# Performance work log

Hardware: AMD Instinct MI355X
Metric: run time of the kernel (lower is better)

The kernel has to match this reference:

```python
import jax
import jax.numpy as jnp
import numpy as np
from jax import lax

TAU = 1.0
EPS = 1e-20


def setup_inputs() -> dict:
    key = jax.random.key(0)
    ks = jax.random.split(key, 8)
    B, n, M, G = 256, 128, 512, 512  # batch, seq, mem_size, global dim
    SLOTS = 15                        # his_mem slots (mem_slots - 1)
    d_q = M + G
    his_mem = jax.random.normal(ks[0], (B, SLOTS, M), dtype=jnp.float32)
    states = jax.random.normal(ks[1], (B, n, M), dtype=jnp.float32)
    states_mask = jnp.round(jax.random.uniform(ks[2], (B, n), dtype=jnp.float32))
    global_trace = jax.random.normal(ks[3], (B, G), dtype=jnp.float32)
    null_mem = jnp.zeros((B, 1, M), dtype=jnp.float32)
    gumbel_u = jax.random.uniform(ks[4], (B, n, SLOTS + 1), dtype=jnp.float32)
    attn_W = jax.random.normal(ks[5], (M, d_q + M), dtype=jnp.float32) * 0.02
    attn_b = jax.random.normal(ks[6], (M,), dtype=jnp.float32) * 0.02
    stdv = 1.0 / np.sqrt(M)
    v = jax.random.normal(ks[7], (M,), dtype=jnp.float32) * stdv
    return {"his_mem": his_mem, "states": states, "states_mask": states_mask,
            "global_trace": global_trace, "null_mem": null_mem,
            "gumbel_u": gumbel_u, "attn_W": attn_W, "attn_b": attn_b, "v": v}


def _gumbel_softmax_hard(logits, u, tau):
    # deterministic gumbel noise from uniform samples u in [0,1)
    g = -jnp.log(-jnp.log(jnp.clip(u, EPS, 1.0)) + EPS)
    y_soft = jax.nn.softmax((logits + g) / tau, axis=-1)
    y_hard = jax.nn.one_hot(jnp.argmax(y_soft, axis=-1), logits.shape[-1],
                            dtype=y_soft.dtype)
    # straight-through estimator (matches torch F.gumbel_softmax hard=True)
    return y_hard - lax.stop_gradient(y_soft) + y_soft


def _forward(his_mem, states, states_mask, global_trace, null_mem,
             gumbel_u, attn_W, attn_b, v):
    B, n, M = states.shape
    S = his_mem.shape[1] + 1  # mem_slots (including null slot)

    def step(hm, xs):
        state, mask, u = xs  # [B,M], [B], [B,S]
        mem = jnp.concatenate([hm, null_mem], axis=1)          # [B,S,M]
        query = jnp.concatenate([state, global_trace], axis=1)  # [B,d_q]
        q = jnp.broadcast_to(query[:, None, :], (B, S, query.shape[-1]))
        energy = jnp.tanh(jnp.concatenate([q, mem], axis=2) @ attn_W.T + attn_b)
        attn_energies = energy @ v                              # [B,S]
        attn_weights = jax.nn.softmax(attn_energies, axis=-1)
        empty_mask = (jnp.sum(jnp.abs(mem), axis=-1) == 0).astype(attn_weights.dtype)
        attn_weights = attn_weights + empty_mask * 10.0
        slot_select = _gumbel_softmax_hard(attn_weights, u, TAU)  # [B,S]
        write_mask = (slot_select[:, : S - 1] * mask[:, None])[:, :, None]  # [B,S-1,1]
        hm = (1.0 - write_mask) * hm + write_mask * state[:, None, :]
        return hm, slot_select

    xs = (jnp.swapaxes(states, 0, 1),        # [n,B,M]
          jnp.swapaxes(states_mask, 0, 1),   # [n,B]
          jnp.swapaxes(gumbel_u, 0, 1))      # [n,B,S]
    hm_final, log = lax.scan(step, his_mem, xs)
    write_log = jnp.swapaxes(log, 0, 1)      # [B,n,S]
    return hm_final, write_log


def reference(his_mem, states, states_mask, global_trace, null_mem,
              gumbel_u, attn_W, attn_b, v):
    return _forward(his_mem, states, states_mask, global_trace, null_mem,
                    gumbel_u, attn_W, attn_b, v)
```

## Files before the change

### kernel.cpp

```cpp
#include <hip/hip_runtime.h>

constexpr int kB = 256;
constexpr int kN = 128;
constexpr int kM = 512;
constexpr int kSlots = 15;
constexpr int kS = 16;
constexpr int kW = 1536;
constexpr int kCap = 8192;

__device__ __forceinline__ float tanh_fast(float x)
{
    float xc = fminf(15.f, fmaxf(-15.f, x));
    float ex = __expf(2.f * xc);
    return 1.f - 2.f * __builtin_amdgcn_rcpf(ex + 1.f);
}

__global__ __launch_bounds__(256) void prep1_k(
    const float* __restrict__ his_mem, const float* __restrict__ null_mem,
    const float* __restrict__ gumbel_u, float* __restrict__ out,
    int* __restrict__ empty0, int* __restrict__ cnt, int* __restrict__ total,
    unsigned* __restrict__ list, int* __restrict__ listPos,
    int* __restrict__ ambBatch, unsigned char* __restrict__ amb_flags)
{
    const int b = blockIdx.x;
    const int tid = threadIdx.x;
    const int wave = tid >> 6, lane = tid & 63;
    __shared__ int eflag[kS];
    float* out_hm = out;
    float* out_log = out + (size_t)kB * kSlots * kM;

    for (int s = wave; s < kS; s += 4) {
        const float* p = (s < kSlots) ? his_mem + (size_t)(b * kSlots + s) * kM
                                      : null_mem + (size_t)b * kM;
        float4 v0 = *(const float4*)(p + lane * 4);
        float4 v1 = *(const float4*)(p + 256 + lane * 4);
        int nz = (v0.x != 0.f) | (v0.y != 0.f) | (v0.z != 0.f) | (v0.w != 0.f) |
                 (v1.x != 0.f) | (v1.y != 0.f) | (v1.z != 0.f) | (v1.w != 0.f);
        unsigned long long bal = __ballot(nz);
        if (lane == 0) eflag[s] = (bal == 0ull) ? 1 : 0;
        if (s < kSlots) {
            float* dst = out_hm + (size_t)(b * kSlots + s) * kM;
            *(float4*)(dst + lane * 4) = v0;
            *(float4*)(dst + 256 + lane * 4) = v1;
        }
    }
    __syncthreads();
    if (tid < kS) empty0[b * kS + tid] = eflag[tid];

    if (tid < kN) {
        const int idx = b * kN + tid;
        const float* up = gumbel_u + (size_t)idx * kS;
        float g[kS];
#pragma unroll
        for (int s = 0; s < kS; ++s) {
            float u = fminf(fmaxf(up[s], 1e-20f), 1.0f);
            g[s] = -logf(-logf(u) + 1e-20f);
        }
        float rhs = g[15] + 10.f * (eflag[15] ? 1.f : 0.f) - 1.01f;
        bool amb = false;
#pragma unroll
        for (int s = 0; s < kSlots; ++s)
            amb = amb || (g[s] + 10.f * (eflag[s] ? 1.f : 0.f) >= rhs);
        amb_flags[idx] = amb ? 1 : 0;
        if (amb) {
            int pos = atomicAdd(&total[0], 1);
            if (pos < kCap) list[pos] = (unsigned)idx;
            listPos[idx] = pos;
            int prev = atomicAdd(&cnt[b], 1);
            if (prev == 0) {
                int bp = atomicAdd(&total[1], 1);
                ambBatch[bp] = b;
            }
        }
        float* lp = out_log + (size_t)idx * kS;
        float4 zz = make_float4(0.f, 0.f, 0.f, 0.f);
        *(float4*)(lp + 0) = zz;
        *(float4*)(lp + 4) = zz;
        *(float4*)(lp + 8) = zz;
        *(float4*)(lp + 12) = make_float4(0.f, 0.f, 0.f, 1.f);
    }
}

__global__ __launch_bounds__(256) void prep2_k(
    const float* __restrict__ W, const float* __restrict__ his_mem,
    const float* __restrict__ null_mem, const float* __restrict__ states,
    const float* __restrict__ global_trace, const float* __restrict__ attn_b,
    const int* __restrict__ total, const int* __restrict__ ambBatch,
    const unsigned* __restrict__ list, float* __restrict__ C0,
    float* __restrict__ qCache, float* __restrict__ cwCache,
    int* __restrict__ stepNz)
{
    const int tid = threadIdx.x;

    if (blockIdx.x < 512) {
        const int nab = total[1];
        const int cx = blockIdx.x >> 3;
        const int cy = blockIdx.x & 7;
        if (cx * 4 >= nab) return;
        __shared__ float As[16 * 68];
        __shared__ float Bs[16 * 68];
        const int n0 = cy * 64;
        const int row_l = tid >> 2;
        const int k4 = (tid & 3) * 4;
        const int ty = tid >> 4, tx = tid & 15;

        int bi = cx * 4 + (row_l >> 4);
        if (bi >= nab) bi = nab - 1;
        const int b = ambBatch[bi];
        const int s = row_l & 15;
        const float* ap = (s < kSlots) ? (his_mem + (size_t)(b * kSlots + s) * kM)
                                       : (null_mem + (size_t)b * kM);
        const float* wp = W + (size_t)(n0 + row_l) * kW + 1024;

        float acc[4][4];
#pragma unroll
        for (int i = 0; i < 4; ++i)
#pragma unroll
            for (int j = 0; j < 4; ++j) acc[i][j] = 0.f;

        for (int kt = 0; kt < kM; kt += 16) {
            float4 a4 = *(const float4*)(ap + kt + k4);
            float4 b4 = *(const float4*)(wp + kt + k4);
            __syncthreads();
            As[(k4 + 0) * 68 + row_l] = a4.x; As[(k4 + 1) * 68 + row_l] = a4.y;
            As[(k4 + 2) * 68 + row_l] = a4.z; As[(k4 + 3) * 68 + row_l] = a4.w;
            Bs[(k4 + 0) * 68 + row_l] = b4.x; Bs[(k4 + 1) * 68 + row_l] = b4.y;
            Bs[(k4 + 2) * 68 + row_l] = b4.z; Bs[(k4 + 3) * 68 + row_l] = b4.w;
            __syncthreads();
#pragma unroll
            for (int k = 0; k < 16; ++k) {
                const float4 av = *(const float4*)&As[k * 68 + ty * 4];
                const float4 bv = *(const float4*)&Bs[k * 68 + tx * 4];
                acc[0][0] = fmaf(av.x, bv.x, acc[0][0]);
                acc[0][1] = fmaf(av.x, bv.y, acc[0][1]);
                acc[0][2] = fmaf(av.x, bv.z, acc[0][2]);
                acc[0][3] = fmaf(av.x, bv.w, acc[0][3]);
                acc[1][0] = fmaf(av.y, bv.x, acc[1][0]);
                acc[1][1] = fmaf(av.y, bv.y, acc[1][1]);
                acc[1][2] = fmaf(av.y, bv.z, acc[1][2]);
                acc[1][3] = fmaf(av.y, bv.w, acc[1][3]);
                acc[2][0] = fmaf(av.z, bv.x, acc[2][0]);
                acc[2][1] = fmaf(av.z, bv.y, acc[2][1]);
                acc[2][2] = fmaf(av.z, bv.z, acc[2][2]);
                acc[2][3] = fmaf(av.z, bv.w, acc[2][3]);
                acc[3][0] = fmaf(av.w, bv.x, acc[3][0]);
                acc[3][1] = fmaf(av.w, bv.y, acc[3][1]);
                acc[3][2] = fmaf(av.w, bv.z, acc[3][2]);
                acc[3][3] = fmaf(av.w, bv.w, acc[3][3]);
            }
        }
#pragma unroll
        for (int i = 0; i < 4; ++i) {
            int rl = ty * 4 + i;
            int bij = cx * 4 + (rl >> 4);
            if (bij >= nab) bij = nab - 1;
            int ro = ambBatch[bij] * kS + (rl & 15);
            float4 o = make_float4(acc[i][0], acc[i][1], acc[i][2], acc[i][3]);
            *(float4*)(C0 + (size_t)ro * kM + n0 + tx * 4) = o;
        }
    } else {
        int n = total[0];
        if (n > kCap) n = kCap;
        __shared__ float Xs[1024];
        __shared__ int nzs;

        for (int c = (int)blockIdx.x - 512; c < n * 16; c += 2048) {
            const int i = c >> 4;
            const int j = c & 15;
            const int idx = (int)list[i];
            const int b = idx >> 7;
            __syncthreads();
            if (tid == 0) nzs = 0;
            __syncthreads();
            float s0 = states[(size_t)idx * kM + tid];
            float s1 = states[(size_t)idx * kM + 256 + tid];
            Xs[tid] = s0; Xs[256 + tid] = s1;
            Xs[512 + tid] = global_trace[(size_t)b * kM + tid];
            Xs[768 + tid] = global_trace[(size_t)b * kM + 256 + tid];
            if (s0 != 0.f || s1 != 0.f) nzs = 1;
            __syncthreads();

            const int g = tid >> 4;
            const int l = tid & 15;
#pragma unroll
            for (int p = 0; p < 2; ++p) {
                const int r = j * 32 + p * 16 + g;
                const float* wr = W + (size_t)r * kW;
                float accq = 0.f, accc = 0.f;
#pragma unroll
                for (int jj = 0; jj < 16; ++jj) {
                    int k = l * 4 + jj * 64;
                    float4 w4 = *(const float4*)(wr + k);
                    float4 x4 = *(const float4*)&Xs[k];
                    accq = fmaf(w4.x, x4.x, accq); accq = fmaf(w4.y, x4.y, accq);
                    accq = fmaf(w4.z, x4.z, accq); accq = fmaf(w4.w, x4.w, accq);
                }
#pragma unroll
                for (int jj = 0; jj < 8; ++jj) {
                    int k = l * 4 + jj * 64;
                    float4 w4 = *(const float4*)(wr + 1024 + k);
                    float4 x4 = *(const float4*)&Xs[k];
                    accc = fmaf(w4.x, x4.x, accc); accc = fmaf(w4.y, x4.y, accc);
                    accc = fmaf(w4.z, x4.z, accc); accc = fmaf(w4.w, x4.w, accc);
                }
                accq += __shfl_xor(accq, 1); accq += __shfl_xor(accq, 2);
                accq += __shfl_xor(accq, 4); accq += __shfl_xor(accq, 8);
                accc += __shfl_xor(accc, 1); accc += __shfl_xor(accc, 2);
                accc += __shfl_xor(accc, 4); accc += __shfl_xor(accc, 8);
                if (l == 0) {
                    qCache[(size_t)i * kM + r] = accq + attn_b[r];
                    cwCache[(size_t)i * kM + r] = accc;
                }
            }
            if (tid == 0 && j == 0) stepNz[i] = nzs;
        }
    }
}

constexpr int kCsStride = 528;

__global__ __launch_bounds__(256) void phaseB_k(
    const float* __restrict__ C0, const int* __restrict__ empty0,
    const unsigned char* __restrict__ amb_flags, const int* __restrict__ cnt,
    const int* __restrict__ listPos, const float* __restrict__ qCache,
    const float* __restrict__ cwCache, const int* __restrict__ stepNz,
    const float* __restrict__ states, const float* __restrict__ states_mask,
    const float* __restrict__ gumbel_u, const float* __restrict__ global_trace,
    const float* __restrict__ W, const float* __restrict__ attn_b,
    const float* __restrict__ v, float* __restrict__ out)
{
    const int b = blockIdx.x;
    if (cnt[b] == 0) return;
    const int tid = threadIdx.x;
    float* out_hm = out;
    float* out_log = out + (size_t)kB * kSlots * kM;

    __shared__ float Cs[kS * kCsStride];
    __shared__ float Xb[1024];
    __shared__ float Qb[kM];
    __shared__ float vs[kM];
    __shared__ float e_sh[kS];
    __shared__ float empty_sh[kS];
    __shared__ unsigned char flS[kN];
    __shared__ int slot_src[kSlots];
    __shared__ int k_sh, wk_sh, nz_sh;

    for (int i = tid; i < kS * kM; i += 256) {
        int s = i >> 9, m = i & 511;
        Cs[s * kCsStride + m] = C0[(size_t)(b * kS + s) * kM + m];
    }
    for (int i = tid; i < kM; i += 256) {
        vs[i] = v[i];
        Xb[512 + i] = global_trace[(size_t)b * kM + i];
    }
    if (tid < kS) empty_sh[tid] = empty0[b * kS + tid] ? 1.0f : 0.0f;
    if (tid < kSlots) slot_src[tid] = -1;
    if (tid < kN) flS[tid] = amb_flags[b * kN + tid];
    __syncthreads();

    const int sidx = tid >> 4;
    const int ml = tid & 15;

    for (int t = 0; t < kN; ++t) {
        if (!flS[t]) continue;

        const int pos = listPos[b * kN + t];
        const float* qp;
        if (pos < kCap) {
            qp = qCache + (size_t)pos * kM;
        } else {
            Xb[tid] = states[(size_t)(b * kN + t) * kM + tid];
            Xb[256 + tid] = states[(size_t)(b * kN + t) * kM + 256 + tid];
            __syncthreads();
            const int g2 = tid >> 4, l2 = tid & 15;
            for (int r0 = 0; r0 < kM; r0 += 16) {
                int r = r0 + g2;
                const float* wr = W + (size_t)r * kW;
                float a = 0.f;
                for (int k = l2 * 4; k < 1024; k += 64) {
                    float4 w4 = *(const float4*)(wr + k);
                    float4 x4 = *(const float4*)&Xb[k];
                    a = fmaf(w4.x, x4.x, a); a = fmaf(w4.y, x4.y, a);
                    a = fmaf(w4.z, x4.z, a); a = fmaf(w4.w, x4.w, a);
                }
                a += __shfl_xor(a, 1); a += __shfl_xor(a, 2);
                a += __shfl_xor(a, 4); a += __shfl_xor(a, 8);
                if (l2 == 0) Qb[r] = a + attn_b[r];
            }
            __syncthreads();
            qp = Qb;
        }

        const float* crow = &Cs[sidx * kCsStride];
        float acc = 0.f;
#pragma unroll
        for (int j = 0; j < 8; ++j) {
            int m = ml * 4 + j * 64;
            float4 q4 = *(const float4*)(qp + m);
            float4 c4 = *(const float4*)&crow[m];
            float4 v4 = *(const float4*)&vs[m];
            acc = fmaf(v4.x, tanh_fast(q4.x + c4.x), acc);
            acc = fmaf(v4.y, tanh_fast(q4.y + c4.y), acc);
            acc = fmaf(v4.z, tanh_fast(q4.z + c4.z), acc);
            acc = fmaf(v4.w, tanh_fast(q4.w + c4.w), acc);
        }
        acc += __shfl_xor(acc, 1); acc += __shfl_xor(acc, 2);
        acc += __shfl_xor(acc, 4); acc += __shfl_xor(acc, 8);
        if (ml == 0) e_sh[sidx] = acc;
        __syncthreads();

        if (tid < 64) {
            int s = tid;
            float ev = (s < kS) ? e_sh[s] : -3.0e38f;
            float mx = ev;
            mx = fmaxf(mx, __shfl_xor(mx, 1));
            mx = fmaxf(mx, __shfl_xor(mx, 2));
            mx = fmaxf(mx, __shfl_xor(mx, 4));
            mx = fmaxf(mx, __shfl_xor(mx, 8));
            float w = (s < kS) ? __expf(ev - mx) : 0.f;
            float sm = w;
            sm += __shfl_xor(sm, 1); sm += __shfl_xor(sm, 2);
            sm += __shfl_xor(sm, 4); sm += __shfl_xor(sm, 8);
            w = w / sm;
            w += 10.0f * ((s < kS) ? empty_sh[s] : 0.f);
            float z;
            if (s < kS) {
                float u = gumbel_u[(size_t)(b * kN + t) * kS + s];
                u = fminf(fmaxf(u, 1e-20f), 1.0f);
                float g = -logf(-logf(u) + 1e-20f);
                z = w + g;
            } else z = -3.0e38f;
            float zm = z;
            zm = fmaxf(zm, __shfl_xor(zm, 1));
            zm = fmaxf(zm, __shfl_xor(zm, 2));
            zm = fmaxf(zm, __shfl_xor(zm, 4));
            zm = fmaxf(zm, __shfl_xor(zm, 8));
            unsigned long long bal = __ballot(z == zm) & 0xFFFFull;
            if (s == 0) k_sh = __ffsll(bal) - 1;
        }
        __syncthreads();

        const int k = k_sh;
        if (tid < kS) out_log[(size_t)(b * kN + t) * kS + tid] = (tid == k) ? 1.f : 0.f;
        if (tid == 0) {
            float mv = states_mask[b * kN + t];
            wk_sh = (k < kSlots && mv != 0.0f) ? k : -1;
            nz_sh = 0;
        }
        __syncthreads();

        const int wk = wk_sh;
        if (wk >= 0) {
            if (pos < kCap) {
                Cs[wk * kCsStride + tid] = cwCache[(size_t)pos * kM + tid];
                Cs[wk * kCsStride + 256 + tid] = cwCache[(size_t)pos * kM + 256 + tid];
                if (tid == 0) {
                    slot_src[wk] = t;
                    empty_sh[wk] = stepNz[pos] ? 0.f : 1.f;
                }
            } else {
                if (Xb[tid] != 0.f || Xb[256 + tid] != 0.f) nz_sh = 1;
                __syncthreads();
                const int g2 = tid >> 4, l2 = tid & 15;
                for (int r0 = 0; r0 < kM; r0 += 16) {
                    int r = r0 + g2;
                    const float* wr = W + (size_t)r * kW + 1024;
                    float ca = 0.f;
                    for (int k2 = l2 * 4; k2 < kM; k2 += 64) {
                        float4 w4 = *(const float4*)(wr + k2);
                        float4 x4 = *(const float4*)&Xb[k2];
                        ca = fmaf(w4.x, x4.x, ca); ca = fmaf(w4.y, x4.y, ca);
                        ca = fmaf(w4.z, x4.z, ca); ca = fmaf(w4.w, x4.w, ca);
                    }
                    ca += __shfl_xor(ca, 1); ca += __shfl_xor(ca, 2);
                    ca += __shfl_xor(ca, 4); ca += __shfl_xor(ca, 8);
                    if (l2 == 0) Cs[wk * kCsStride + r] = ca;
                }
                __syncthreads();
                if (tid == 0) {
                    slot_src[wk] = t;
                    empty_sh[wk] = nz_sh ? 0.f : 1.f;
                }
            }
        }
        __syncthreads();
    }

    for (int s = 0; s < kSlots; ++s) {
        int ts = slot_src[s];
        if (ts >= 0) {
            float* dst = out_hm + (size_t)(b * kSlots + s) * kM;
            dst[tid] = states[(size_t)(b * kN + ts) * kM + tid];
            dst[tid + 256] = states[(size_t)(b * kN + ts) * kM + tid + 256];
        }
    }
}

extern "C" void kernel_launch(void* const* d_in, const int* in_sizes, int n_in,
                              void* d_out, int out_size, void* d_ws, size_t ws_size,
                              hipStream_t stream)
{
    const float* his_mem      = (const float*)d_in[0];
    const float* states       = (const float*)d_in[1];
    const float* states_mask  = (const float*)d_in[2];
    const float* global_trace = (const float*)d_in[3];
    const float* null_mem     = (const float*)d_in[4];
    const float* gumbel_u     = (const float*)d_in[5];
    const float* attn_W       = (const float*)d_in[6];
    const float* attn_b       = (const float*)d_in[7];
    const float* v            = (const float*)d_in[8];

    float* C0 = (float*)d_ws;
    float* qCache = C0 + (size_t)kB * kS * kM;
    float* cwCache = qCache + (size_t)kCap * kM;
    int* cnt = (int*)(cwCache + (size_t)kCap * kM);
    int* total = cnt + kB;
    int* empty0 = total + 16;
    int* ambBatch = empty0 + kB * kS;
    int* stepNz = ambBatch + kB;
    int* listPos = stepNz + kCap;
    unsigned* list = (unsigned*)(listPos + kB * kN);
    unsigned char* amb = (unsigned char*)(list + kB * kN);

    hipMemsetAsync(cnt, 0, (kB + 16) * sizeof(int), stream);
    prep1_k<<<kB, 256, 0, stream>>>(his_mem, null_mem, gumbel_u, (float*)d_out,
                                    empty0, cnt, total, list, listPos, ambBatch,
                                    amb);
    prep2_k<<<2560, 256, 0, stream>>>(attn_W, his_mem, null_mem, states,
                                      global_trace, attn_b, total, ambBatch,
                                      list, C0, qCache, cwCache, stepNz);
    phaseB_k<<<kB, 256, 0, stream>>>(C0, empty0, amb, cnt, listPos, qCache,
                                     cwCache, stepNz, states, states_mask,
                                     gumbel_u, global_trace, attn_W, attn_b, v,
                                     (float*)d_out);
}
```

Measured before the change: 170.4 us.

## Fuse prep kernels and sequential scan into one per-batch kernel

Collapses the three-kernel pipeline (memset, prep1, batched GEMM/precompute prep2, sequential phaseB) into a single kernel with one block per batch element. Each block builds its ambiguous-step list in shared memory via ballots instead of global atomics. It computes the memory-projection C0 from shared-memory copies of the slots, and computes the query and written-slot projections inline per ambiguous step rather than caching them in global workspace. This removes launch overhead and global round trips, but puts all per-step matvec work on only 256 blocks in sequence rather than spreading it across a wide parallel grid.

```diff
diff --git a/kernel.cpp b/kernel.cpp
--- a/kernel.cpp
+++ b/kernel.cpp
@@ -6,7 +6,8 @@
 constexpr int kSlots = 15;
 constexpr int kS = 16;
 constexpr int kW = 1536;
-constexpr int kCap = 8192;
+constexpr int kMsStride = 520;
+constexpr int kCsStride = 528;
 
 __device__ __forceinline__ float tanh_fast(float x)
 {
@@ -15,38 +16,53 @@
     return 1.f - 2.f * __builtin_amdgcn_rcpf(ex + 1.f);
 }
 
-__global__ __launch_bounds__(256) void prep1_k(
-    const float* __restrict__ his_mem, const float* __restrict__ null_mem,
-    const float* __restrict__ gumbel_u, float* __restrict__ out,
-    int* __restrict__ empty0, int* __restrict__ cnt, int* __restrict__ total,
-    unsigned* __restrict__ list, int* __restrict__ listPos,
-    int* __restrict__ ambBatch, unsigned char* __restrict__ amb_flags)
+__global__ __launch_bounds__(256) void fused_k(
+    const float* __restrict__ his_mem, const float* __restrict__ states,
+    const float* __restrict__ states_mask, const float* __restrict__ global_trace,
+    const float* __restrict__ null_mem, const float* __restrict__ gumbel_u,
+    const float* __restrict__ W, const float* __restrict__ attn_b,
+    const float* __restrict__ v, float* __restrict__ out)
 {
     const int b = blockIdx.x;
     const int tid = threadIdx.x;
     const int wave = tid >> 6, lane = tid & 63;
-    __shared__ int eflag[kS];
+
+    __shared__ __align__(16) float Ms[kS * kMsStride];
+    __shared__ __align__(16) float Cs[kS * kCsStride];
+    __shared__ __align__(16) float Xq[1024];
+    __shared__ __align__(16) float Qs[kM];
+    __shared__ __align__(16) float vs[kM];
+    __shared__ __align__(16) float bs[kM];
+    __shared__ float empty_p[kS];
+    __shared__ float e_sh[kS];
+    __shared__ unsigned char ambList[kN];
+    __shared__ int wcnt[2];
+    __shared__ int slot_src[kSlots];
+    __shared__ int cnt_sh, k_sh, wk_sh, nz_sh;
+
     float* out_hm = out;
     float* out_log = out + (size_t)kB * kSlots * kM;
 
     for (int s = wave; s < kS; s += 4) {
-        const float* p = (s < kSlots) ? his_mem + (size_t)(b * kSlots + s) * kM
+        const float* p = (s < kSlots) ? his_mem + ((size_t)b * kSlots + s) * kM
                                       : null_mem + (size_t)b * kM;
         float4 v0 = *(const float4*)(p + lane * 4);
         float4 v1 = *(const float4*)(p + 256 + lane * 4);
+        *(float4*)&Ms[s * kMsStride + lane * 4] = v0;
+        *(float4*)&Ms[s * kMsStride + 256 + lane * 4] = v1;
         int nz = (v0.x != 0.f) | (v0.y != 0.f) | (v0.z != 0.f) | (v0.w != 0.f) |
                  (v1.x != 0.f) | (v1.y != 0.f) | (v1.z != 0.f) | (v1.w != 0.f);
         unsigned long long bal = __ballot(nz);
-        if (lane == 0) eflag[s] = (bal == 0ull) ? 1 : 0;
+        if (lane == 0) empty_p[s] = (bal == 0ull) ? 1.f : 0.f;
         if (s < kSlots) {
-            float* dst = out_hm + (size_t)(b * kSlots + s) * kM;
+            float* dst = out_hm + ((size_t)b * kSlots + s) * kM;
             *(float4*)(dst + lane * 4) = v0;
             *(float4*)(dst + 256 + lane * 4) = v1;
         }
     }
     __syncthreads();
-    if (tid < kS) empty0[b * kS + tid] = eflag[tid];
-
+
+    bool amb = false;
     if (tid < kN) {
         const int idx = b * kN + tid;
         const float* up = gumbel_u + (size_t)idx * kS;
@@ -56,22 +72,10 @@
             float u = fminf(fmaxf(up[s], 1e-20f), 1.0f);
             g[s] = -logf(-logf(u) + 1e-20f);
         }
-        float rhs = g[15] + 10.f * (eflag[15] ? 1.f : 0.f) - 1.01f;
-        bool amb = false;
+        float rhs = g[15] + 10.f * empty_p[15] - 1.01f;
 #pragma unroll
         for (int s = 0; s < kSlots; ++s)
-            amb = amb || (g[s] + 10.f * (eflag[s] ? 1.f : 0.f) >= rhs);
-        amb_flags[idx] = amb ? 1 : 0;
-        if (amb) {
-            int pos = atomicAdd(&total[0], 1);
-            if (pos < kCap) list[pos] = (unsigned)idx;
-            listPos[idx] = pos;
-            int prev = atomicAdd(&cnt[b], 1);
-            if (prev == 0) {
-                int bp = atomicAdd(&total[1], 1);
-                ambBatch[bp] = b;
-            }
-        }
+            amb = amb || (g[s] + 10.f * empty_p[s] >= rhs);
         float* lp = out_log + (size_t)idx * kS;
         float4 zz = make_float4(0.f, 0.f, 0.f, 0.f);
         *(float4*)(lp + 0) = zz;
@@ -79,234 +83,124 @@
         *(float4*)(lp + 8) = zz;
         *(float4*)(lp + 12) = make_float4(0.f, 0.f, 0.f, 1.f);
     }
-}
-
-__global__ __launch_bounds__(256) void prep2_k(
-    const float* __restrict__ W, const float* __restrict__ his_mem,
-    const float* __restrict__ null_mem, const float* __restrict__ states,
-    const float* __restrict__ global_trace, const float* __restrict__ attn_b,
-    const int* __restrict__ total, const int* __restrict__ ambBatch,
-    const unsigned* __restrict__ list, float* __restrict__ C0,
-    float* __restrict__ qCache, float* __restrict__ cwCache,
-    int* __restrict__ stepNz)
-{
-    const int tid = threadIdx.x;
-
-    if (blockIdx.x < 512) {
-        const int nab = total[1];
-        const int cx = blockIdx.x >> 3;
-        const int cy = blockIdx.x & 7;
-        if (cx * 4 >= nab) return;
-        __shared__ float As[16 * 68];
-        __shared__ float Bs[16 * 68];
-        const int n0 = cy * 64;
-        const int row_l = tid >> 2;
-        const int k4 = (tid & 3) * 4;
-        const int ty = tid >> 4, tx = tid & 15;
-
-        int bi = cx * 4 + (row_l >> 4);
-        if (bi >= nab) bi = nab - 1;
-        const int b = ambBatch[bi];
-        const int s = row_l & 15;
-        const float* ap = (s < kSlots) ? (his_mem + (size_t)(b * kSlots + s) * kM)
-                                       : (null_mem + (size_t)b * kM);
-        const float* wp = W + (size_t)(n0 + row_l) * kW + 1024;
-
-        float acc[4][4];
-#pragma unroll
-        for (int i = 0; i < 4; ++i)
-#pragma unroll
-            for (int j = 0; j < 4; ++j) acc[i][j] = 0.f;
-
-        for (int kt = 0; kt < kM; kt += 16) {
-            float4 a4 = *(const float4*)(ap + kt + k4);
-            float4 b4 = *(const float4*)(wp + kt + k4);
-            __syncthreads();
-            As[(k4 + 0) * 68 + row_l] = a4.x; As[(k4 + 1) * 68 + row_l] = a4.y;
-            As[(k4 + 2) * 68 + row_l] = a4.z; As[(k4 + 3) * 68 + row_l] = a4.w;
-            Bs[(k4 + 0) * 68 + row_l] = b4.x; Bs[(k4 + 1) * 68 + row_l] = b4.y;
-            Bs[(k4 + 2) * 68 + row_l] = b4.z; Bs[(k4 + 3) * 68 + row_l] = b4.w;
-            __syncthreads();
-#pragma unroll
-            for (int k = 0; k < 16; ++k) {
-                const float4 av = *(const float4*)&As[k * 68 + ty * 4];
-                const float4 bv = *(const float4*)&Bs[k * 68 + tx * 4];
-                acc[0][0] = fmaf(av.x, bv.x, acc[0][0]);
-                acc[0][1] = fmaf(av.x, bv.y, acc[0][1]);
-                acc[0][2] = fmaf(av.x, bv.z, acc[0][2]);
-                acc[0][3] = fmaf(av.x, bv.w, acc[0][3]);
-                acc[1][0] = fmaf(av.y, bv.x, acc[1][0]);
-                acc[1][1] = fmaf(av.y, bv.y, acc[1][1]);
-                acc[1][2] = fmaf(av.y, bv.z, acc[1][2]);
-                acc[1][3] = fmaf(av.y, bv.w, acc[1][3]);
-                acc[2][0] = fmaf(av.z, bv.x, acc[2][0]);
-                acc[2][1] = fmaf(av.z, bv.y, acc[2][1]);
-                acc[2][2] = fmaf(av.z, bv.z, acc[2][2]);
-                acc[2][3] = fmaf(av.z, bv.w, acc[2][3]);
-                acc[3][0] = fmaf(av.w, bv.x, acc[3][0]);
-                acc[3][1] = fmaf(av.w, bv.y, acc[3][1]);
-                acc[3][2] = fmaf(av.w, bv.z, acc[3][2]);
-                acc[3][3] = fmaf(av.w, bv.w, acc[3][3]);
-            }
-        }
-#pragma unroll
-        for (int i = 0; i < 4; ++i) {
-            int rl = ty * 4 + i;
-            int bij = cx * 4 + (rl >> 4);
-            if (bij >= nab) bij = nab - 1;
-            int ro = ambBatch[bij] * kS + (rl & 15);
-            float4 o = make_float4(acc[i][0], acc[i][1], acc[i][2], acc[i][3]);
-            *(float4*)(C0 + (size_t)ro * kM + n0 + tx * 4) = o;
-        }
-    } else {
-        int n = total[0];
-        if (n > kCap) n = kCap;
-        __shared__ float Xs[1024];
-        __shared__ int nzs;
-
-        for (int c = (int)blockIdx.x - 512; c < n * 16; c += 2048) {
-            const int i = c >> 4;
-            const int j = c & 15;
-            const int idx = (int)list[i];
-            const int b = idx >> 7;
-            __syncthreads();
-            if (tid == 0) nzs = 0;
-            __syncthreads();
+    unsigned long long m = __ballot(amb);
+    if (tid < kN && (tid & 63) == 0) wcnt[tid >> 6] = __popcll(m);
+    __syncthreads();
+    if (tid < kN && amb) {
+        int base = (tid >= 64) ? wcnt[0] : 0;
+        int pos = base + __popcll(m & ((1ull << (tid & 63)) - 1ull));
+        ambList[pos] = (unsigned char)tid;
+    }
+    if (tid == 0) cnt_sh = wcnt[0] + wcnt[1];
+    if (tid < kSlots) slot_src[tid] = -1;
+    __syncthreads();
+    const int cnt = cnt_sh;
+    if (cnt == 0) return;
+
+    for (int i = tid; i < kM; i += 256) {
+        vs[i] = v[i];
+        bs[i] = attn_b[i];
+        Xq[512 + i] = global_trace[(size_t)b * kM + i];
+    }
+
+    {
+        const int g = tid >> 4, l = tid & 15;
+        const int koff = l * 4;
+        float4 w4[8];
+        {
+            const float* wr = W + (size_t)g * kW + 1024;
+#pragma unroll
+            for (int jj = 0; jj < 8; ++jj)
+                w4[jj] = *(const float4*)(wr + koff + jj * 64);
+        }
+        for (int r0 = 0; r0 < kM; r0 += 16) {
+            float4 wn[8];
+            if (r0 + 16 < kM) {
+                const float* wr = W + (size_t)(r0 + 16 + g) * kW + 1024;
+#pragma unroll
+                for (int jj = 0; jj < 8; ++jj)
+                    wn[jj] = *(const float4*)(wr + koff + jj * 64);
+            }
+            const int r = r0 + g;
+#pragma unroll
+            for (int s = 0; s < kS; ++s) {
+                const float* ms = &Ms[s * kMsStride + koff];
+                float a0 = 0.f, a1 = 0.f, a2 = 0.f, a3 = 0.f;
+#pragma unroll
+                for (int jj = 0; jj < 8; ++jj) {
+                    float4 m4 = *(const float4*)(ms + jj * 64);
+                    a0 = fmaf(w4[jj].x, m4.x, a0);
+                    a1 = fmaf(w4[jj].y, m4.y, a1);
+                    a2 = fmaf(w4[jj].z, m4.z, a2);
+                    a3 = fmaf(w4[jj].w, m4.w, a3);
+                }
+                float a = (a0 + a1) + (a2 + a3);
+                a += __shfl_xor(a, 1); a += __shfl_xor(a, 2);
+                a += __shfl_xor(a, 4); a += __shfl_xor(a, 8);
+                if (l == s) Cs[s * kCsStride + r] = a;
+            }
+#pragma unroll
+            for (int jj = 0; jj < 8; ++jj) w4[jj] = wn[jj];
+        }
+    }
+    __syncthreads();
+
+    const int sidx = tid >> 4;
+    const int ml = tid & 15;
+    const int g = tid >> 4, l = tid & 15;
+    const int koff = l * 4;
+
+    for (int jj = 0; jj < cnt; ++jj) {
+        const int t = ambList[jj];
+        const int idx = b * kN + t;
+
+        if (tid == 0) nz_sh = 0;
+        __syncthreads();
+        {
             float s0 = states[(size_t)idx * kM + tid];
             float s1 = states[(size_t)idx * kM + 256 + tid];
-            Xs[tid] = s0; Xs[256 + tid] = s1;
-            Xs[512 + tid] = global_trace[(size_t)b * kM + tid];
-            Xs[768 + tid] = global_trace[(size_t)b * kM + 256 + tid];
-            if (s0 != 0.f || s1 != 0.f) nzs = 1;
-            __syncthreads();
-
-            const int g = tid >> 4;
-            const int l = tid & 15;
-#pragma unroll
-            for (int p = 0; p < 2; ++p) {
-                const int r = j * 32 + p * 16 + g;
-                const float* wr = W + (size_t)r * kW;
-                float accq = 0.f, accc = 0.f;
-#pragma unroll
-                for (int jj = 0; jj < 16; ++jj) {
-                    int k = l * 4 + jj * 64;
-                    float4 w4 = *(const float4*)(wr + k);
-                    float4 x4 = *(const float4*)&Xs[k];
-                    accq = fmaf(w4.x, x4.x, accq); accq = fmaf(w4.y, x4.y, accq);
-                    accq = fmaf(w4.z, x4.z, accq); accq = fmaf(w4.w, x4.w, accq);
-                }
-#pragma unroll
-                for (int jj = 0; jj < 8; ++jj) {
-                    int k = l * 4 + jj * 64;
-                    float4 w4 = *(const float4*)(wr + 1024 + k);
-                    float4 x4 = *(const float4*)&Xs[k];
-                    accc = fmaf(w4.x, x4.x, accc); accc = fmaf(w4.y, x4.y, accc);
-                    accc = fmaf(w4.z, x4.z, accc); accc = fmaf(w4.w, x4.w, accc);
-                }
-                accq += __shfl_xor(accq, 1); accq += __shfl_xor(accq, 2);
-                accq += __shfl_xor(accq, 4); accq += __shfl_xor(accq, 8);
-                accc += __shfl_xor(accc, 1); accc += __shfl_xor(accc, 2);
-                accc += __shfl_xor(accc, 4); accc += __shfl_xor(accc, 8);
-                if (l == 0) {
-                    qCache[(size_t)i * kM + r] = accq + attn_b[r];
-                    cwCache[(size_t)i * kM + r] = accc;
-                }
-            }
-            if (tid == 0 && j == 0) stepNz[i] = nzs;
-        }
-    }
-}
-
-constexpr int kCsStride = 528;
-
-__global__ __launch_bounds__(256) void phaseB_k(
-    const float* __restrict__ C0, const int* __restrict__ empty0,
-    const unsigned char* __restrict__ amb_flags, const int* __restrict__ cnt,
-    const int* __restrict__ listPos, const float* __restrict__ qCache,
-    const float* __restrict__ cwCache, const int* __restrict__ stepNz,
-    const float* __restrict__ states, const float* __restrict__ states_mask,
-    const float* __restrict__ gumbel_u, const float* __restrict__ global_trace,
-    const float* __restrict__ W, const float* __restrict__ attn_b,
-    const float* __restrict__ v, float* __restrict__ out)
-{
-    const int b = blockIdx.x;
-    if (cnt[b] == 0) return;
-    const int tid = threadIdx.x;
-    float* out_hm = out;
-    float* out_log = out + (size_t)kB * kSlots * kM;
-
-    __shared__ float Cs[kS * kCsStride];
-    __shared__ float Xb[1024];
-    __shared__ float Qb[kM];
-    __shared__ float vs[kM];
-    __shared__ float e_sh[kS];
-    __shared__ float empty_sh[kS];
-    __shared__ unsigned char flS[kN];
-    __shared__ int slot_src[kSlots];
-    __shared__ int k_sh, wk_sh, nz_sh;
-
-    for (int i = tid; i < kS * kM; i += 256) {
-        int s = i >> 9, m = i & 511;
-        Cs[s * kCsStride + m] = C0[(size_t)(b * kS + s) * kM + m];
-    }
-    for (int i = tid; i < kM; i += 256) {
-        vs[i] = v[i];
-        Xb[512 + i] = global_trace[(size_t)b * kM + i];
-    }
-    if (tid < kS) empty_sh[tid] = empty0[b * kS + tid] ? 1.0f : 0.0f;
-    if (tid < kSlots) slot_src[tid] = -1;
-    if (tid < kN) flS[tid] = amb_flags[b * kN + tid];
-    __syncthreads();
-
-    const int sidx = tid >> 4;
-    const int ml = tid & 15;
-
-    for (int t = 0; t < kN; ++t) {
-        if (!flS[t]) continue;
-
-        const int pos = listPos[b * kN + t];
-        const float* qp;
-        if (pos < kCap) {
-            qp = qCache + (size_t)pos * kM;
-        } else {
-            Xb[tid] = states[(size_t)(b * kN + t) * kM + tid];
-            Xb[256 + tid] = states[(size_t)(b * kN + t) * kM + 256 + tid];
-            __syncthreads();
-            const int g2 = tid >> 4, l2 = tid & 15;
-            for (int r0 = 0; r0 < kM; r0 += 16) {
-                int r = r0 + g2;
-                const float* wr = W + (size_t)r * kW;
-                float a = 0.f;
-                for (int k = l2 * 4; k < 1024; k += 64) {
-                    float4 w4 = *(const float4*)(wr + k);
-                    float4 x4 = *(const float4*)&Xb[k];
-                    a = fmaf(w4.x, x4.x, a); a = fmaf(w4.y, x4.y, a);
-                    a = fmaf(w4.z, x4.z, a); a = fmaf(w4.w, x4.w, a);
-                }
-                a += __shfl_xor(a, 1); a += __shfl_xor(a, 2);
-                a += __shfl_xor(a, 4); a += __shfl_xor(a, 8);
-                if (l2 == 0) Qb[r] = a + attn_b[r];
-            }
-            __syncthreads();
-            qp = Qb;
-        }
-
-        const float* crow = &Cs[sidx * kCsStride];
-        float acc = 0.f;
-#pragma unroll
-        for (int j = 0; j < 8; ++j) {
-            int m = ml * 4 + j * 64;
-            float4 q4 = *(const float4*)(qp + m);
-            float4 c4 = *(const float4*)&crow[m];
-            float4 v4 = *(const float4*)&vs[m];
-            acc = fmaf(v4.x, tanh_fast(q4.x + c4.x), acc);
-            acc = fmaf(v4.y, tanh_fast(q4.y + c4.y), acc);
-            acc = fmaf(v4.z, tanh_fast(q4.z + c4.z), acc);
-            acc = fmaf(v4.w, tanh_fast(q4.w + c4.w), acc);
-        }
-        acc += __shfl_xor(acc, 1); acc += __shfl_xor(acc, 2);
-        acc += __shfl_xor(acc, 4); acc += __shfl_xor(acc, 8);
-        if (ml == 0) e_sh[sidx] = acc;
+            Xq[tid] = s0; Xq[256 + tid] = s1;
+            if (s0 != 0.f || s1 != 0.f) nz_sh = 1;
+        }
+        __syncthreads();
+
+#pragma unroll 2
+        for (int r0 = 0; r0 < kM; r0 += 16) {
+            const int r = r0 + g;
+            const float* wr = W + (size_t)r * kW;
+            float a0 = 0.f, a1 = 0.f, a2 = 0.f, a3 = 0.f;
+#pragma unroll
+            for (int q = 0; q < 16; ++q) {
+                float4 wv = *(const float4*)(wr + koff + q * 64);
+                float4 xv = *(const float4*)&Xq[koff + q * 64];
+                a0 = fmaf(wv.x, xv.x, a0); a1 = fmaf(wv.y, xv.y, a1);
+                a2 = fmaf(wv.z, xv.z, a2); a3 = fmaf(wv.w, xv.w, a3);
+            }
+            float a = (a0 + a1) + (a2 + a3);
+            a += __shfl_xor(a, 1); a += __shfl_xor(a, 2);
+            a += __shfl_xor(a, 4); a += __shfl_xor(a, 8);
+            if (l == 0) Qs[r] = a + bs[r];
+        }
+        __syncthreads();
+
+        {
+            const float* crow = &Cs[sidx * kCsStride];
+            float acc = 0.f;
+#pragma unroll
+            for (int j = 0; j < 8; ++j) {
+                int mcol = ml * 4 + j * 64;
+                float4 q4 = *(const float4*)&Qs[mcol];
+                float4 c4 = *(const float4*)&crow[mcol];
+                float4 v4 = *(const float4*)&vs[mcol];
+                acc = fmaf(v4.x, tanh_fast(q4.x + c4.x), acc);
+                acc = fmaf(v4.y, tanh_fast(q4.y + c4.y), acc);
+                acc = fmaf(v4.z, tanh_fast(q4.z + c4.z), acc);
+                acc = fmaf(v4.w, tanh_fast(q4.w + c4.w), acc);
+            }
+            acc += __shfl_xor(acc, 1); acc += __shfl_xor(acc, 2);
+            acc += __shfl_xor(acc, 4); acc += __shfl_xor(acc, 8);
+            if (ml == 0) e_sh[sidx] = acc;
+        }
         __syncthreads();
 
         if (tid < 64) {
@@ -322,13 +216,13 @@
             sm += __shfl_xor(sm, 1); sm += __shfl_xor(sm, 2);
             sm += __shfl_xor(sm, 4); sm += __shfl_xor(sm, 8);
             w = w / sm;
-            w += 10.0f * ((s < kS) ? empty_sh[s] : 0.f);
+            w += 10.0f * ((s < kS) ? empty_p[s] : 0.f);
             float z;
             if (s < kS) {
-                float u = gumbel_u[(size_t)(b * kN + t) * kS + s];
+                float u = gumbel_u[(size_t)idx * kS + s];
                 u = fminf(fmaxf(u, 1e-20f), 1.0f);
-                float g = -logf(-logf(u) + 1e-20f);
-                z = w + g;
+                float gn = -logf(-logf(u) + 1e-20f);
+                z = w + gn;
             } else z = -3.0e38f;
             float zm = z;
             zm = fmaxf(zm, __shfl_xor(zm, 1));
@@ -341,46 +235,35 @@
         __syncthreads();
 
         const int k = k_sh;
-        if (tid < kS) out_log[(size_t)(b * kN + t) * kS + tid] = (tid == k) ? 1.f : 0.f;
+        if (tid < kS)
+            out_log[(size_t)idx * kS + tid] = (tid == k) ? 1.f : 0.f;
         if (tid == 0) {
-            float mv = states_mask[b * kN + t];
+            float mv = states_mask[idx];
             wk_sh = (k < kSlots && mv != 0.0f) ? k : -1;
-            nz_sh = 0;
         }
         __syncthreads();
 
         const int wk = wk_sh;
         if (wk >= 0) {
-            if (pos < kCap) {
-                Cs[wk * kCsStride + tid] = cwCache[(size_t)pos * kM + tid];
-                Cs[wk * kCsStride + 256 + tid] = cwCache[(size_t)pos * kM + 256 + tid];
-                if (tid == 0) {
-                    slot_src[wk] = t;
-                    empty_sh[wk] = stepNz[pos] ? 0.f : 1.f;
+            for (int r0 = 0; r0 < kM; r0 += 16) {
+                const int r = r0 + g;
+                const float* wr = W + (size_t)r * kW + 1024;
+                float a0 = 0.f, a1 = 0.f, a2 = 0.f, a3 = 0.f;
+#pragma unroll
+                for (int q = 0; q < 8; ++q) {
+                    float4 wv = *(const float4*)(wr + koff + q * 64);
+                    float4 xv = *(const float4*)&Xq[koff + q * 64];
+                    a0 = fmaf(wv.x, xv.x, a0); a1 = fmaf(wv.y, xv.y, a1);
+                    a2 = fmaf(wv.z, xv.z, a2); a3 = fmaf(wv.w, xv.w, a3);
                 }
-            } else {
-                if (Xb[tid] != 0.f || Xb[256 + tid] != 0.f) nz_sh = 1;
-                __syncthreads();
-                const int g2 = tid >> 4, l2 = tid & 15;
-                for (int r0 = 0; r0 < kM; r0 += 16) {
-                    int r = r0 + g2;
-                    const float* wr = W + (size_t)r * kW + 1024;
-                    float ca = 0.f;
-                    for (int k2 = l2 * 4; k2 < kM; k2 += 64) {
-                        float4 w4 = *(const float4*)(wr + k2);
-                        float4 x4 = *(const float4*)&Xb[k2];
-                        ca = fmaf(w4.x, x4.x, ca); ca = fmaf(w4.y, x4.y, ca);
-                        ca = fmaf(w4.z, x4.z, ca); ca = fmaf(w4.w, x4.w, ca);
-                    }
-                    ca += __shfl_xor(ca, 1); ca += __shfl_xor(ca, 2);
-                    ca += __shfl_xor(ca, 4); ca += __shfl_xor(ca, 8);
-                    if (l2 == 0) Cs[wk * kCsStride + r] = ca;
-                }
-                __syncthreads();
-                if (tid == 0) {
-                    slot_src[wk] = t;
-                    empty_sh[wk] = nz_sh ? 0.f : 1.f;
-                }
+                float a = (a0 + a1) + (a2 + a3);
+                a += __shfl_xor(a, 1); a += __shfl_xor(a, 2);
+                a += __shfl_xor(a, 4); a += __shfl_xor(a, 8);
+                if (l == 0) Cs[wk * kCsStride + r] = a;
+            }
+            if (tid == 0) {
+                slot_src[wk] = t;
+                empty_p[wk] = nz_sh ? 0.f : 1.f;
             }
         }
         __syncthreads();
@@ -389,9 +272,9 @@
     for (int s = 0; s < kSlots; ++s) {
         int ts = slot_src[s];
         if (ts >= 0) {
-            float* dst = out_hm + (size_t)(b * kSlots + s) * kM;
-            dst[tid] = states[(size_t)(b * kN + ts) * kM + tid];
-            dst[tid + 256] = states[(size_t)(b * kN + ts) * kM + tid + 256];
+            float* dst = out_hm + ((size_t)b * kSlots + s) * kM;
+            dst[tid] = states[((size_t)b * kN + ts) * kM + tid];
+            dst[tid + 256] = states[((size_t)b * kN + ts) * kM + tid + 256];
         }
     }
 }
@@ -410,27 +293,7 @@
     const float* attn_b       = (const float*)d_in[7];
     const float* v            = (const float*)d_in[8];
 
-    float* C0 = (float*)d_ws;
-    float* qCache = C0 + (size_t)kB * kS * kM;
-    float* cwCache = qCache + (size_t)kCap * kM;
-    int* cnt = (int*)(cwCache + (size_t)kCap * kM);
-    int* total = cnt + kB;
-    int* empty0 = total + 16;
-    int* ambBatch = empty0 + kB * kS;
-    int* stepNz = ambBatch + kB;
-    int* listPos = stepNz + kCap;
-    unsigned* list = (unsigned*)(listPos + kB * kN);
-    unsigned char* amb = (unsigned char*)(list + kB * kN);
-
-    hipMemsetAsync(cnt, 0, (kB + 16) * sizeof(int), stream);
-    prep1_k<<<kB, 256, 0, stream>>>(his_mem, null_mem, gumbel_u, (float*)d_out,
-                                    empty0, cnt, total, list, listPos, ambBatch,
-                                    amb);
-    prep2_k<<<2560, 256, 0, stream>>>(attn_W, his_mem, null_mem, states,
-                                      global_trace, attn_b, total, ambBatch,
-                                      list, C0, qCache, cwCache, stepNz);
-    phaseB_k<<<kB, 256, 0, stream>>>(C0, empty0, amb, cnt, listPos, qCache,
-                                     cwCache, stepNz, states, states_mask,
-                                     gumbel_u, global_trace, attn_W, attn_b, v,
-                                     (float*)d_out);
+    fused_k<<<kB, 256, 0, stream>>>(his_mem, states, states_mask, global_trace,
+                                    null_mem, gumbel_u, attn_W, attn_b, v,
+                                    (float*)d_out);
 }
```

Measured after the change: 345.7 us. 2.03x slower.
